# Kernel tuning notes

Hardware: AMD Instinct MI355X
Metric: run time of the kernel (lower is better)

The kernel has to match this reference:

```python
import jax, jax.numpy as jnp
import numpy as np


def setup_inputs() -> dict:
    key = jax.random.key(0)
    k1, k2, k3, k4 = jax.random.split(key, 4)
    B, D, N, M = 4, 256, 4096, 4096
    return {
        "src": jax.random.normal(k1, (B, 3, N), dtype=jnp.float32),
        "tgt": jax.random.normal(k2, (B, 3, M), dtype=jnp.float32),
        "src_emb": jax.random.normal(k3, (B, D, N), dtype=jnp.float32),
        "tgt_emb": jax.random.normal(k4, (B, D, M), dtype=jnp.float32),
    }


def reference(src, tgt, src_emb, tgt_emb):
    # pairwise_distance[b,n,m] = -||src_emb[:,n] - tgt_emb[:,m]||^2
    # decomposed as -xx + 2*inner - yy (inner below is -2*dot, as in torch code)
    inner = -2.0 * jnp.einsum("bdn,bdm->bnm", src_emb, tgt_emb)       # [B,N,M]
    xx = jnp.sum(src_emb ** 2, axis=1)[:, :, None]                     # [B,N,1]
    yy = jnp.sum(tgt_emb ** 2, axis=1)[:, None, :]                     # [B,1,M]
    pairwise_distance = -xx - inner - yy                               # [B,N,M]
    scores = jax.nn.softmax(pairwise_distance, axis=2)                 # softmax over tgt points
    # src_corr[b,c,n] = sum_m tgt[b,c,m] * scores[b,n,m]
    src_corr = jnp.einsum("bcm,bnm->bcn", tgt, scores)                 # [B,3,N]
    return src_corr
```

## Files before the change

kernel.cpp:

```cpp
#include <hip/hip_runtime.h>

#define NBATCH 4
#define DDIM   256
#define NN     4096
#define MM     4096
#define NCHUNK 8
#define MCHUNK 512
#define MTILE  32
#define LOG2E  1.44269504088896340736f

using half4   = __attribute__((ext_vector_type(4))) _Float16;
using half8   = __attribute__((ext_vector_type(8))) _Float16;
using floatx4 = __attribute__((ext_vector_type(4))) float;


__global__ __launch_bounds__(256) void k_prep(const float* __restrict__ src_emb,
                                              const float* __restrict__ tgt_emb,
                                              const float* __restrict__ tgt,
                                              _Float16* __restrict__ Qf,
                                              _Float16* __restrict__ Kf,
                                              float* __restrict__ yyS,
                                              float4* __restrict__ Vt) {
    __shared__ __align__(16) float tile[128 * 64];
    __shared__ float psum[4][64];
    int i = blockIdx.x;
    int tensor = i & 1, b = (i >> 1) & 3, dg = (i >> 3) & 1, ng = i >> 4;
    int t = threadIdx.x, w = t >> 6, lane = t & 63;
    const float* in = tensor ? tgt_emb : src_emb;
    _Float16* outp  = tensor ? Kf : Qf;
    const float scale = tensor ? 1.0f : 2.0f * LOG2E;

    const char* gb = (const char*)(in + ((size_t)b * DDIM + dg * 128 + w * 32) * NN + ng * 64);
    char* lb = (char*)tile + w * 8192;
#pragma unroll
    for (int it = 0; it < 8; it++) {
        __builtin_amdgcn_global_load_lds(
            (const __attribute__((address_space(1))) uint32_t*)(const void*)
                (gb + (size_t)(it * 4 + (lane >> 4)) * (NN * 4) + (lane & 15) * 16),
            (__attribute__((address_space(3))) uint32_t*)(void*)
                (lb + it * 1024),
            16, 0, 0);
    }
    __syncthreads();

    float ss = 0.f;
    half8* ob = (half8*)(outp + (size_t)b * NN * DDIM);
    int n_glob = ng * 64 + lane;
    int blk = n_glob >> 4, l15 = n_glob & 15;
#pragma unroll
    for (int q = 0; q < 4; q++) {
        int octg = w * 4 + q;
        half8 v;
#pragma unroll
        for (int k = 0; k < 8; k++) {
            float f = tile[(octg * 8 + k) * 64 + lane];
            ss = fmaf(f, f, ss);
            v[k] = (_Float16)(f * scale);
        }
        int dglob = dg * 128 + octg * 8;
        int dsg = dglob >> 5, oct = (dglob >> 3) & 3;
        ob[(((size_t)blk * 8 + dsg) * 4 + oct) * 16 + l15] = v;
    }
    if (tensor) {
        psum[w][lane] = ss;
        __syncthreads();
        if (t < 64) {
            float s = (psum[0][t] + psum[1][t]) + (psum[2][t] + psum[3][t]);
            s *= -LOG2E;
            int m = ng * 64 + t;
            if (dg == 0) {
                const float* tp = tgt + (size_t)b * 3 * MM + m;
                Vt[(size_t)b * MM + m] = make_float4(tp[0], tp[MM], tp[2 * MM], s);
            } else {
                yyS[(size_t)b * MM + m] = s;
            }
        }
    }
}

__global__ __launch_bounds__(256, 2) void k_flash(const _Float16* __restrict__ Qf,
                                                  const _Float16* __restrict__ Kf,
                                                  const float* __restrict__ yyS,
                                                  const float4* __restrict__ Vt,
                                                  float4* __restrict__ Opart,
                                                  float* __restrict__ Mpart) {
    __shared__ __align__(16) _Float16 Kt[2][MTILE * DDIM];
    __shared__ __align__(8)  half4 vh[MCHUNK];
    __shared__ __align__(16) float yyt[MCHUNK];

    int i = blockIdx.x, t = threadIdx.x;
    int xcd = i & 7, j = i >> 3;
    int b = xcd >> 1, nhalf = xcd & 1;
    int chunk = j & 7, ntile = nhalf * 16 + (j >> 3);

    int wave = t >> 6, lane = t & 63, quad = lane >> 4, l15 = lane & 15;
    int m0 = chunk * MCHUNK;
    int mblk0 = m0 >> 4;

    const char* kfb = (const char*)(Kf + (size_t)b * NN * DDIM);
    auto stage = [&](int mt) {
        const char* gb = kfb + (size_t)(mblk0 + mt * 2) * 8192 + wave * 4096;
        char* lb = (char*)&Kt[mt & 1][0] + wave * 4096;
#pragma unroll
        for (int it = 0; it < 4; it++) {
            __builtin_amdgcn_global_load_lds(
                (const __attribute__((address_space(1))) uint32_t*)(const void*)
                    (gb + it * 1024 + lane * 16),
                (__attribute__((address_space(3))) uint32_t*)(void*)
                    (lb + it * 1024),
            16, 0, 0);
        }
    };

    stage(0);

    {
        const float4* vb = Vt + (size_t)b * MM + m0;
        const float* yb = yyS + (size_t)b * MM + m0;
        for (int r = t; r < MCHUNK; r += 256) {
            float4 g = vb[r];
            half4 h; h[0] = (_Float16)g.x; h[1] = (_Float16)g.y;
            h[2] = (_Float16)g.z; h[3] = (_Float16)0.f;
            vh[r] = h;
            yyt[r] = g.w + yb[r];
        }
    }

    int nblk0 = ntile * 8 + wave * 2;
    const half8* qp = (const half8*)Qf + (size_t)b * NN * 32;
    half8 qf[2][8];
#pragma unroll
    for (int nb = 0; nb < 2; nb++)
#pragma unroll
        for (int ds = 0; ds < 8; ds++)
            qf[nb][ds] = qp[(((size_t)(nblk0 + nb) * 8 + ds) * 4 + quad) * 16 + l15];
#pragma unroll
    for (int nb = 0; nb < 2; nb++)
#pragma unroll
        for (int ds = 0; ds < 8; ds++)
            asm volatile("" : "+v"(qf[nb][ds]));

    stage(1);

    asm volatile("s_waitcnt vmcnt(4)" ::: "memory");
    asm volatile("s_barrier" ::: "memory");

    const floatx4 z4 = {0.f, 0.f, 0.f, 0.f};
    floatx4 o[2] = {z4, z4};
    float mr[2] = {-__builtin_inff(), -__builtin_inff()};

    for (int mt = 0; mt < MCHUNK / MTILE; mt++) {
        const char* Kb = (const char*)&Kt[mt & 1][0];
        int vbase = mt * MTILE;
        floatx4 yv0 = *(const floatx4*)&yyt[vbase + quad * 4];
        floatx4 yv1 = *(const floatx4*)&yyt[vbase + 16 + quad * 4];
        floatx4 acc[2][2] = {{yv0, yv0}, {yv1, yv1}};
        __builtin_amdgcn_s_setprio(1);
#pragma unroll
        for (int mb = 0; mb < 2; mb++) {
            const char* rb = Kb + mb * 8192 + lane * 16;
#pragma unroll
            for (int ds = 0; ds < 8; ds++) {
                half8 a = *(const half8*)(rb + ds * 1024);
                acc[mb][0] = __builtin_amdgcn_mfma_f32_16x16x32_f16(a, qf[0][ds], acc[mb][0], 0, 0, 0);
                acc[mb][1] = __builtin_amdgcn_mfma_f32_16x16x32_f16(a, qf[1][ds], acc[mb][1], 0, 0, 0);
            }
        }
        __builtin_amdgcn_s_setprio(0);

#pragma unroll
        for (int nb = 0; nb < 2; nb++) {
            float tm = fmaxf(fmaxf(fmaxf(acc[0][nb][0], acc[0][nb][1]),
                                   fmaxf(acc[0][nb][2], acc[0][nb][3])),
                             fmaxf(fmaxf(acc[1][nb][0], acc[1][nb][1]),
                                   fmaxf(acc[1][nb][2], acc[1][nb][3])));
            if (__any(tm > mr[nb])) {
                float mn = fmaxf(mr[nb], tm);
                float al = __builtin_amdgcn_exp2f(mr[nb] - mn);
                mr[nb] = mn;
                o[nb] = o[nb] * al;
            }
        }
#pragma unroll
        for (int jj = 0; jj < 8; jj++) {
            half4 vrh = vh[vbase + (jj >> 2) * 16 + quad * 4 + (jj & 3)];
            float v0 = (float)vrh[0], v1 = (float)vrh[1], v2 = (float)vrh[2];
#pragma unroll
            for (int nb = 0; nb < 2; nb++) {
                float p = __builtin_amdgcn_exp2f(acc[jj >> 2][nb][jj & 3] - mr[nb]);
                o[nb][0] = fmaf(p, v0, o[nb][0]);
                o[nb][1] = fmaf(p, v1, o[nb][1]);
                o[nb][2] = fmaf(p, v2, o[nb][2]);
                o[nb][3] += p;
            }
        }

        if (mt < MCHUNK / MTILE - 1) {
            asm volatile("s_barrier" ::: "memory");
            if (mt + 2 < MCHUNK / MTILE) {
                stage(mt + 2);
                asm volatile("s_waitcnt vmcnt(4)" ::: "memory");
            } else {
                asm volatile("s_waitcnt vmcnt(0)" ::: "memory");
            }
            asm volatile("s_barrier" ::: "memory");
        }
    }

#pragma unroll
    for (int nb = 0; nb < 2; nb++) {
        float mq = mr[nb];
        float ma = fmaxf(mq, __shfl_xor(mq, 16, 64));
        ma = fmaxf(ma, __shfl_xor(ma, 32, 64));
        float wgt = __builtin_amdgcn_exp2f(mq - ma);
        floatx4 ow = o[nb] * wgt;
#pragma unroll
        for (int c = 0; c < 4; c++) {
            float v = ow[c];
            v += __shfl_xor(v, 16, 64);
            v += __shfl_xor(v, 32, 64);
            ow[c] = v;
        }
        if (quad == 0) {
            int n = (nblk0 + nb) * 16 + l15;
            size_t idx = (size_t)(chunk * NBATCH + b) * NN + n;
            Opart[idx] = make_float4(ow[0], ow[1], ow[2], ow[3]);
            Mpart[idx] = ma;
        }
    }
}

__global__ __launch_bounds__(128) void k_combine(const float4* __restrict__ Opart,
                                                 const float* __restrict__ Mpart,
                                                 float* __restrict__ out) {
    int idx = blockIdx.x * 128 + threadIdx.x;
    int b = idx >> 12, n = idx & (NN - 1);
    float mstar = -__builtin_inff();
#pragma unroll
    for (int j = 0; j < NCHUNK; j++)
        mstar = fmaxf(mstar, Mpart[(size_t)(j * NBATCH + b) * NN + n]);
    float o0 = 0.f, o1 = 0.f, o2 = 0.f, l = 0.f;
#pragma unroll
    for (int j = 0; j < NCHUNK; j++) {
        size_t id = (size_t)(j * NBATCH + b) * NN + n;
        float w = __builtin_amdgcn_exp2f(Mpart[id] - mstar);
        float4 P = Opart[id];
        o0 = fmaf(w, P.x, o0); o1 = fmaf(w, P.y, o1);
        o2 = fmaf(w, P.z, o2); l  = fmaf(w, P.w, l);
    }
    out[(size_t)(b * 3 + 0) * NN + n] = o0 / l;
    out[(size_t)(b * 3 + 1) * NN + n] = o1 / l;
    out[(size_t)(b * 3 + 2) * NN + n] = o2 / l;
}

extern "C" void kernel_launch(void* const* d_in, const int* in_sizes, int n_in,
                              void* d_out, int out_size, void* d_ws, size_t ws_size,
                              hipStream_t stream) {
    const float* tgt     = (const float*)d_in[1];
    const float* src_emb = (const float*)d_in[2];
    const float* tgt_emb = (const float*)d_in[3];
    float* out = (float*)d_out;

    char* ws = (char*)d_ws;
    _Float16* Qf  = (_Float16*)(ws);
    _Float16* Kf  = (_Float16*)(ws + 8388608);
    float*    yyS = (float*)   (ws + 16777216);
    float4*   Vt  = (float4*)  (ws + 16842752);
    float4*   Op  = (float4*)  (ws + 17104896);
    float*    Mp  = (float*)   (ws + 19202048);

    hipLaunchKernelGGL(k_prep,    dim3(1024), dim3(256), 0, stream,
                       src_emb, tgt_emb, tgt, Qf, Kf, yyS, Vt);
    hipLaunchKernelGGL(k_flash,   dim3(1024), dim3(256), 0, stream, Qf, Kf, yyS, Vt, Op, Mp);
    hipLaunchKernelGGL(k_combine, dim3(128),  dim3(128), 0, stream, Op, Mp, out);
}
```

Baseline: 129.0 us.

## Fuse split-M combine into flash kernel via last-block atomic counter

Removes the separate combine kernel launch. Each flash block signals completion with an atomic counter per (batch, n-tile), and the last of the eight chunk blocks merges the partial outputs and writes the final result. The counter is reset inside the prep kernel. This saves one launch and its tail, at the cost of a threadfence, an atomic and a serialized combine tail in the last-arriving blocks.

```diff
diff --git a/kernel.cpp b/kernel.cpp
--- a/kernel.cpp
+++ b/kernel.cpp
@@ -12,6 +12,8 @@
 using half4   = __attribute__((ext_vector_type(4))) _Float16;
 using half8   = __attribute__((ext_vector_type(8))) _Float16;
 using floatx4 = __attribute__((ext_vector_type(4))) float;
+
+__device__ int g_cnt[NBATCH * 32];
 
 
 __global__ __launch_bounds__(256) void k_prep(const float* __restrict__ src_emb,
@@ -24,6 +26,7 @@
     __shared__ __align__(16) float tile[128 * 64];
     __shared__ float psum[4][64];
     int i = blockIdx.x;
+    if (i == 0 && threadIdx.x < NBATCH * 32) g_cnt[threadIdx.x] = 0;
     int tensor = i & 1, b = (i >> 1) & 3, dg = (i >> 3) & 1, ng = i >> 4;
     int t = threadIdx.x, w = t >> 6, lane = t & 63;
     const float* in = tensor ? tgt_emb : src_emb;
@@ -83,10 +86,12 @@
                                                   const float* __restrict__ yyS,
                                                   const float4* __restrict__ Vt,
                                                   float4* __restrict__ Opart,
-                                                  float* __restrict__ Mpart) {
+                                                  float* __restrict__ Mpart,
+                                                  float* __restrict__ out) {
     __shared__ __align__(16) _Float16 Kt[2][MTILE * DDIM];
     __shared__ __align__(8)  half4 vh[MCHUNK];
     __shared__ __align__(16) float yyt[MCHUNK];
+    __shared__ int lastflag;
 
     int i = blockIdx.x, t = threadIdx.x;
     int xcd = i & 7, j = i >> 3;
@@ -228,29 +233,36 @@
             Mpart[idx] = ma;
         }
     }
-}
-
-__global__ __launch_bounds__(128) void k_combine(const float4* __restrict__ Opart,
-                                                 const float* __restrict__ Mpart,
-                                                 float* __restrict__ out) {
-    int idx = blockIdx.x * 128 + threadIdx.x;
-    int b = idx >> 12, n = idx & (NN - 1);
-    float mstar = -__builtin_inff();
-#pragma unroll
-    for (int j = 0; j < NCHUNK; j++)
-        mstar = fmaxf(mstar, Mpart[(size_t)(j * NBATCH + b) * NN + n]);
-    float o0 = 0.f, o1 = 0.f, o2 = 0.f, l = 0.f;
-#pragma unroll
-    for (int j = 0; j < NCHUNK; j++) {
-        size_t id = (size_t)(j * NBATCH + b) * NN + n;
-        float w = __builtin_amdgcn_exp2f(Mpart[id] - mstar);
-        float4 P = Opart[id];
-        o0 = fmaf(w, P.x, o0); o1 = fmaf(w, P.y, o1);
-        o2 = fmaf(w, P.z, o2); l  = fmaf(w, P.w, l);
-    }
-    out[(size_t)(b * 3 + 0) * NN + n] = o0 / l;
-    out[(size_t)(b * 3 + 1) * NN + n] = o1 / l;
-    out[(size_t)(b * 3 + 2) * NN + n] = o2 / l;
+
+    __threadfence();
+    __syncthreads();
+    if (t == 0) {
+        int old = atomicAdd(&g_cnt[b * 32 + ntile], 1);
+        lastflag = ((old & (NCHUNK - 1)) == NCHUNK - 1);
+    }
+    __syncthreads();
+    if (lastflag) {
+        __threadfence();
+        if (t < 128) {
+            int n = ntile * 128 + t;
+            float mstar = -__builtin_inff();
+#pragma unroll
+            for (int jc = 0; jc < NCHUNK; jc++)
+                mstar = fmaxf(mstar, Mpart[(size_t)(jc * NBATCH + b) * NN + n]);
+            float o0 = 0.f, o1 = 0.f, o2 = 0.f, l = 0.f;
+#pragma unroll
+            for (int jc = 0; jc < NCHUNK; jc++) {
+                size_t id = (size_t)(jc * NBATCH + b) * NN + n;
+                float w = __builtin_amdgcn_exp2f(Mpart[id] - mstar);
+                float4 P = Opart[id];
+                o0 = fmaf(w, P.x, o0); o1 = fmaf(w, P.y, o1);
+                o2 = fmaf(w, P.z, o2); l  = fmaf(w, P.w, l);
+            }
+            out[(size_t)(b * 3 + 0) * NN + n] = o0 / l;
+            out[(size_t)(b * 3 + 1) * NN + n] = o1 / l;
+            out[(size_t)(b * 3 + 2) * NN + n] = o2 / l;
+        }
+    }
 }
 
 extern "C" void kernel_launch(void* const* d_in, const int* in_sizes, int n_in,
@@ -269,8 +281,8 @@
     float4*   Op  = (float4*)  (ws + 17104896);
     float*    Mp  = (float*)   (ws + 19202048);
 
-    hipLaunchKernelGGL(k_prep,    dim3(1024), dim3(256), 0, stream,
+    hipLaunchKernelGGL(k_prep,  dim3(1024), dim3(256), 0, stream,
                        src_emb, tgt_emb, tgt, Qf, Kf, yyS, Vt);
-    hipLaunchKernelGGL(k_flash,   dim3(1024), dim3(256), 0, stream, Qf, Kf, yyS, Vt, Op, Mp);
-    hipLaunchKernelGGL(k_combine, dim3(128),  dim3(128), 0, stream, Op, Mp, out);
+    hipLaunchKernelGGL(k_flash, dim3(1024), dim3(256), 0, stream,
+                       Qf, Kf, yyS, Vt, Op, Mp, out);
 }
```

Result: slower. 202.6 us (+57.1%).
